# Kernel tuning notes

Measured on AMD Instinct MI355X. Metric: run time of the kernel, lower is better.

The kernel has to match this reference:

```python
import jax, jax.numpy as jnp
import numpy as np

D = 1024  # input_dim == output_dim
B = 4096  # batch (acts as sequence for batch-wise self-attention)


def setup_inputs() -> dict:
    key = jax.random.key(0)
    k1, k2, k3, k4 = jax.random.split(key, 4)
    inputs = jax.random.normal(k1, (B, D), dtype=jnp.float32)
    rotation_params = jax.random.normal(k2, (D, D), dtype=jnp.float32)
    # torch nn.Linear(input_dim, output_dim): weight (out, in), bias (out,)
    linear_w = jax.random.normal(k3, (D, D), dtype=jnp.float32) * (1.0 / np.sqrt(D))
    linear_b = jax.random.normal(k4, (D,), dtype=jnp.float32) * 0.01
    return {"inputs": inputs, "rotation_params": rotation_params,
            "linear_w": linear_w, "linear_b": linear_b}


def reference(inputs, rotation_params, linear_w, linear_b):
    # query = X R ; key = X R^T  -> scores = softmax(Q K^T / sqrt(D)) over batch dim
    query = inputs @ rotation_params                 # [B, D]
    key = inputs @ rotation_params.T                 # [B, D]
    scale = 1.0 / np.sqrt(D).astype(np.float32)
    scores = jax.nn.softmax(jnp.einsum('bd,cd->bc', query, key) * scale, axis=-1)  # [B, B]
    weighted = scores @ inputs                        # [B, D]
    return weighted @ linear_w.T + linear_b           # [B, out]
```

## Files before the change

### kernel.cpp

```cpp
#include <hip/hip_runtime.h>
#include <math.h>
#include <stdint.h>

using f16 = _Float16;
using half8 = __attribute__((ext_vector_type(8))) f16;
using half4 = __attribute__((ext_vector_type(4))) f16;
using f32x4 = __attribute__((ext_vector_type(4))) float;

__device__ __forceinline__ void gl_lds16(const f16* g, f16* l) {
  __builtin_amdgcn_global_load_lds(
      (const __attribute__((address_space(1))) void*)g,
      (__attribute__((address_space(3))) void*)l, 16, 0, 0);
}

__global__ __launch_bounds__(512, 2) void gemm_q3(
    const f16* __restrict__ Ap, const f16* __restrict__ Bp,
    f16* __restrict__ Ch, long sCp, int N, int K, long sAp, long sBp,
    float scale) {
  __shared__ f16 lds[2 * 4096 * 8];
  const int tid = threadIdx.x;
  const int lane = tid & 63;
  const int wave = tid >> 6;
  const int wr = (wave >> 2) * 128;
  const int wc = (wave & 3) * 64;

  const int nwg = gridDim.x * gridDim.y;
  int bid = blockIdx.y * gridDim.x + blockIdx.x;
  bid = (bid & 7) * (nwg >> 3) + (bid >> 3);
  const int bm = (bid / gridDim.x) * 256;
  const int bn = (bid % gridDim.x) * 256;

  const int nt = K / 32;

  auto stage = [&](int t, int i) {
    const int g0 = i * 512 + wave * 64;
    const int ga = g0 + lane;
    const bool isB = ga >= 2048;
    const int gl = ga & 2047;
    const int pl = gl >> 10;
    const int gp = gl & 1023;
    const int r = gp >> 2;
    const int cg = (gp & 3) ^ ((r >> 1) & 3);
    const f16* gs = (isB ? Bp + (size_t)pl * sBp + (size_t)(bn + r) * K
                         : Ap + (size_t)pl * sAp + (size_t)(bm + r) * K) +
                    t * 32 + cg * 8;
    gl_lds16(gs, &lds[((size_t)(t & 1) * 4096 + g0) * 8]);
  };

  int aoff[2][8], boff[2][4];
#pragma unroll
  for (int pl = 0; pl < 2; ++pl) {
#pragma unroll
    for (int fr = 0; fr < 8; ++fr) {
      const int row = wr + fr * 16 + (lane & 15);
      const int kg = (lane >> 4) ^ ((row >> 1) & 3);
      aoff[pl][fr] = (pl * 1024 + row * 4 + kg) * 8;
    }
#pragma unroll
    for (int fc = 0; fc < 4; ++fc) {
      const int col = wc + fc * 16 + (lane & 15);
      const int kg = (lane >> 4) ^ ((col >> 1) & 3);
      boff[pl][fc] = (2048 + pl * 1024 + col * 4 + kg) * 8;
    }
  }

  f32x4 acc[8][4];
#pragma unroll
  for (int m = 0; m < 8; ++m)
#pragma unroll
    for (int n = 0; n < 4; ++n) acc[m][n] = (f32x4){0.f, 0.f, 0.f, 0.f};

  half8 af0[2][4], af1[2][4], bf0[2][2], bf1[2][2];

#define LOAD_A(dst, h)                                          \
  _Pragma("unroll") for (int pl = 0; pl < 2; ++pl)              \
      _Pragma("unroll") for (int i = 0; i < 4; ++i) dst[pl][i] = \
          *(const half8*)&buf[aoff[pl][(h) * 4 + i]];
#define LOAD_B(dst, h)                                          \
  _Pragma("unroll") for (int pl = 0; pl < 2; ++pl)              \
      _Pragma("unroll") for (int j = 0; j < 2; ++j) dst[pl][j] = \
          *(const half8*)&buf[boff[pl][(h) * 2 + j]];
#define MFMA_Q(A, B, ah, bh)                                                  \
  _Pragma("unroll") for (int i = 0; i < 4; ++i)                               \
      _Pragma("unroll") for (int j = 0; j < 2; ++j) {                         \
    f32x4& c = acc[(ah) * 4 + i][(bh) * 2 + j];                               \
    c = __builtin_amdgcn_mfma_f32_16x16x32_f16(A[0][i], B[0][j], c, 0, 0, 0); \
    c = __builtin_amdgcn_mfma_f32_16x16x32_f16(A[0][i], B[1][j], c, 0, 0, 0); \
    c = __builtin_amdgcn_mfma_f32_16x16x32_f16(A[1][i], B[0][j], c, 0, 0, 0); \
  }
#define SBAR0() __builtin_amdgcn_sched_barrier(0)

#pragma unroll
  for (int i = 0; i < 8; ++i) stage(0, i);

  for (int t = 0; t < nt; ++t) {
    const f16* buf = &lds[(size_t)(t & 1) * 4096 * 8];
    asm volatile("s_barrier" ::: "memory");
    const bool pf = (t + 1 < nt);
    if (pf) {
      stage(t + 1, 0); stage(t + 1, 1); stage(t + 1, 2); stage(t + 1, 3);
      SBAR0();
      asm volatile("s_waitcnt vmcnt(4)" ::: "memory");
    } else {
      asm volatile("s_waitcnt vmcnt(0)" ::: "memory");
    }
    SBAR0();
    LOAD_A(af0, 0);
    LOAD_B(bf0, 0);
    LOAD_B(bf1, 1);
    SBAR0();
    __builtin_amdgcn_s_setprio(1);
    MFMA_Q(af0, bf0, 0, 0);
    __builtin_amdgcn_s_setprio(0);
    SBAR0();
    LOAD_A(af1, 1);
    if (pf) { stage(t + 1, 4); stage(t + 1, 5); stage(t + 1, 6); stage(t + 1, 7); }
    SBAR0();
    __builtin_amdgcn_s_setprio(1);
    MFMA_Q(af0, bf1, 0, 1);
    __builtin_amdgcn_s_setprio(0);
    SBAR0();
    LOAD_B(bf0, 0);
    SBAR0();
    __builtin_amdgcn_s_setprio(1);
    MFMA_Q(af1, bf1, 1, 1);
    __builtin_amdgcn_s_setprio(0);
    SBAR0();
    __builtin_amdgcn_s_setprio(1);
    MFMA_Q(af1, bf0, 1, 0);
    __builtin_amdgcn_s_setprio(0);
    SBAR0();
  }
#undef LOAD_A
#undef LOAD_B
#undef MFMA_Q
#undef SBAR0

#pragma unroll
  for (int m = 0; m < 8; ++m) {
#pragma unroll
    for (int n = 0; n < 4; ++n) {
      const int col = bn + wc + n * 16 + (lane & 15);
#pragma unroll
      for (int q = 0; q < 4; ++q) {
        const int row = bm + wr + m * 16 + (lane >> 4) * 4 + q;
        const float v = acc[m][n][q] * scale;
        const f16 h = (f16)v;
        Ch[(size_t)row * N + col] = h;
        Ch[sCp + (size_t)row * N + col] = (f16)(v - (float)h);
      }
    }
  }
}

template <int NP, int EPI, bool BIASF>
__global__ __launch_bounds__(512, 2) void gemm_dp(
    const f16* __restrict__ Ap, const f16* __restrict__ Bp,
    void* __restrict__ Cv, const float* __restrict__ bias, int M, int N, int K,
    long sAp, long sBp, long sCp, float scale) {
  __shared__ f16 lds[3 * 2048 * 8];
  const int tid = threadIdx.x;
  const int lane = tid & 63;
  const int wave = tid >> 6;
  const int wr = (wave >> 1) * 32;
  const int wc = (wave & 1) * 64;

  const int nwg = gridDim.x * gridDim.y;
  int bid = blockIdx.y * gridDim.x + blockIdx.x;
  bid = (bid & 7) * (nwg >> 3) + (bid >> 3);
  const int bm = (bid / gridDim.x) * 128;
  const int bn = (bid % gridDim.x) * 128;

  constexpr int KSTEP = (NP == 2) ? 32 : 64;
  const int nt = K / KSTEP;

  auto stage = [&](int t, int i) {
    const int g0 = i * 512 + wave * 64;
    const int ga = g0 + lane;
    const bool isB = ga >= 1024;
    const int gl = ga & 1023;
    const int pl = gl >> 9;
    const int gp = gl & 511;
    const int r = gp >> 2;
    const int cg = (gp & 3) ^ ((r >> 1) & 3);
    const long sP = (NP == 2) ? (isB ? sBp : sAp) : 0;
    const int kOff = (NP == 2) ? 0 : pl * 32;
    const f16* gs = (isB ? Bp : Ap) + (size_t)pl * sP +
                    (size_t)((isB ? bn : bm) + r) * K + t * KSTEP + kOff +
                    cg * 8;
    gl_lds16(gs, &lds[((size_t)(t % 3) * 2048 + g0) * 8]);
  };

  int aoff[2][2], boff[2][4];
#pragma unroll
  for (int pl = 0; pl < 2; ++pl) {
#pragma unroll
    for (int m = 0; m < 2; ++m) {
      const int row = wr + m * 16 + (lane & 15);
      const int kg = (lane >> 4) ^ ((row >> 1) & 3);
      aoff[pl][m] = (pl * 512 + row * 4 + kg) * 8;
    }
#pragma unroll
    for (int n = 0; n < 4; ++n) {
      const int col = wc + n * 16 + (lane & 15);
      const int kg = (lane >> 4) ^ ((col >> 1) & 3);
      boff[pl][n] = (1024 + pl * 512 + col * 4 + kg) * 8;
    }
  }

  f32x4 acc[2][4];
#pragma unroll
  for (int m = 0; m < 2; ++m)
#pragma unroll
    for (int n = 0; n < 4; ++n) acc[m][n] = (f32x4){0.f, 0.f, 0.f, 0.f};

#pragma unroll
  for (int i = 0; i < 4; ++i) stage(0, i);
#pragma unroll
  for (int i = 0; i < 4; ++i) stage(1, i);

  for (int t = 0; t < nt; ++t) {
    const f16* buf = &lds[(size_t)(t % 3) * 2048 * 8];
    if (t + 1 < nt)
      asm volatile("s_waitcnt vmcnt(4)" ::: "memory");
    else
      asm volatile("s_waitcnt vmcnt(0)" ::: "memory");
    asm volatile("s_barrier" ::: "memory");

    half8 af[2][2], b0[2][2];
#pragma unroll
    for (int pl = 0; pl < 2; ++pl) {
#pragma unroll
      for (int m = 0; m < 2; ++m) af[pl][m] = *(const half8*)&buf[aoff[pl][m]];
#pragma unroll
      for (int j = 0; j < 2; ++j) b0[pl][j] = *(const half8*)&buf[boff[pl][j]];
    }
    if (t + 2 < nt) {
      stage(t + 2, 0);
      stage(t + 2, 1);
    }
    __builtin_amdgcn_sched_barrier(0);
    asm volatile("s_barrier" ::: "memory");
    asm volatile("s_waitcnt lgkmcnt(0)" ::: "memory");
    __builtin_amdgcn_sched_barrier(0);
    __builtin_amdgcn_s_setprio(1);
#pragma unroll
    for (int m = 0; m < 2; ++m) {
#pragma unroll
      for (int j = 0; j < 2; ++j) {
        acc[m][j] = __builtin_amdgcn_mfma_f32_16x16x32_f16(af[0][m], b0[0][j],
                                                           acc[m][j], 0, 0, 0);
        if (NP == 2) {
          acc[m][j] = __builtin_amdgcn_mfma_f32_16x16x32_f16(
              af[0][m], b0[1][j], acc[m][j], 0, 0, 0);
          acc[m][j] = __builtin_amdgcn_mfma_f32_16x16x32_f16(
              af[1][m], b0[0][j], acc[m][j], 0, 0, 0);
        } else {
          acc[m][j] = __builtin_amdgcn_mfma_f32_16x16x32_f16(
              af[1][m], b0[1][j], acc[m][j], 0, 0, 0);
        }
      }
    }
    __builtin_amdgcn_s_setprio(0);
    __builtin_amdgcn_sched_barrier(0);
    asm volatile("s_barrier" ::: "memory");

    half8 b1[2][2];
#pragma unroll
    for (int pl = 0; pl < 2; ++pl)
#pragma unroll
      for (int j = 0; j < 2; ++j)
        b1[pl][j] = *(const half8*)&buf[boff[pl][2 + j]];
    if (t + 2 < nt) {
      stage(t + 2, 2);
      stage(t + 2, 3);
    }
    __builtin_amdgcn_sched_barrier(0);
    asm volatile("s_barrier" ::: "memory");
    asm volatile("s_waitcnt lgkmcnt(0)" ::: "memory");
    __builtin_amdgcn_sched_barrier(0);
    __builtin_amdgcn_s_setprio(1);
#pragma unroll
    for (int m = 0; m < 2; ++m) {
#pragma unroll
      for (int j = 0; j < 2; ++j) {
        acc[m][2 + j] = __builtin_amdgcn_mfma_f32_16x16x32_f16(
            af[0][m], b1[0][j], acc[m][2 + j], 0, 0, 0);
        if (NP == 2) {
          acc[m][2 + j] = __builtin_amdgcn_mfma_f32_16x16x32_f16(
              af[0][m], b1[1][j], acc[m][2 + j], 0, 0, 0);
          acc[m][2 + j] = __builtin_amdgcn_mfma_f32_16x16x32_f16(
              af[1][m], b1[0][j], acc[m][2 + j], 0, 0, 0);
        } else {
          acc[m][2 + j] = __builtin_amdgcn_mfma_f32_16x16x32_f16(
              af[1][m], b1[1][j], acc[m][2 + j], 0, 0, 0);
        }
      }
    }
    __builtin_amdgcn_s_setprio(0);
    __builtin_amdgcn_sched_barrier(0);
  }

#pragma unroll
  for (int m = 0; m < 2; ++m) {
#pragma unroll
    for (int n = 0; n < 4; ++n) {
      const int col = bn + wc + n * 16 + (lane & 15);
      const float bv = BIASF ? bias[col] : 0.f;
#pragma unroll
      for (int q = 0; q < 4; ++q) {
        const int row = bm + wr + m * 16 + (lane >> 4) * 4 + q;
        float v = acc[m][n][q] * scale;
        if (EPI == 0) {
          ((float*)Cv)[(size_t)row * N + col] = v + bv;
        } else if (EPI == 1) {
          f16* C = (f16*)Cv;
          const f16 h = (f16)v;
          C[(size_t)row * N + col] = h;
          C[sCp + (size_t)row * N + col] = (f16)(v - (float)h);
        } else {
          ((f16*)Cv)[(size_t)row * N + col] = (f16)v;
        }
      }
    }
  }
}

template <int NP, int TN, int EPI, bool BIASF, int MINW>
__global__ __launch_bounds__(256, MINW) void gemm_mp(
    const f16* __restrict__ Ap, const f16* __restrict__ Bp,
    void* __restrict__ Cv, const float* __restrict__ bias, int M, int N, int K,
    long sAp, long sBp, long sCp, float scale) {
  constexpr int FR = (TN == 128) ? 4 : 2;
  constexpr int FC = 4;
  constexpr int AG = NP * 512;
  constexpr int BPG = TN * 4;
  __shared__ f16 As[NP * 128 * 32];
  __shared__ f16 Bs[NP * TN * 32];
  const int tid = threadIdx.x;
  const int lane = tid & 63;
  const int wave = tid >> 6;
  const int wr = (TN == 128) ? (wave >> 1) * 64 : wave * 32;
  const int wc = (TN == 128) ? (wave & 1) * 64 : 0;

  const int nwg = gridDim.x * gridDim.y;
  int bid = blockIdx.y * gridDim.x + blockIdx.x;
  bid = (bid & 7) * (nwg >> 3) + (bid >> 3);
  const int bm = (bid / gridDim.x) * 128;
  const int bn = (bid % gridDim.x) * TN;

  int aoff[NP][FR], boff[NP][FC];
#pragma unroll
  for (int p = 0; p < NP; ++p) {
#pragma unroll
    for (int m = 0; m < FR; ++m) {
      const int row = wr + m * 16 + (lane & 15);
      const int kga = (lane >> 4) ^ ((row >> 1) & 3);
      aoff[p][m] = (p * 512 + row * 4 + kga) * 8;
    }
#pragma unroll
    for (int n = 0; n < FC; ++n) {
      const int col = wc + n * 16 + (lane & 15);
      const int kgb = (lane >> 4) ^ ((col >> 1) & 3);
      boff[p][n] = (p * BPG + col * 4 + kgb) * 8;
    }
  }

  f32x4 acc[FR][FC];
#pragma unroll
  for (int m = 0; m < FR; ++m)
#pragma unroll
    for (int n = 0; n < FC; ++n) acc[m][n] = (f32x4){0.f, 0.f, 0.f, 0.f};

  for (int k0 = 0; k0 < K; k0 += 32) {
#pragma unroll
    for (int i = 0; i < (NP * (512 + TN * 4)) / 256; ++i) {
      const int g0 = i * 256 + wave * 64;
      const bool isB = g0 >= AG;
      const int ga0 = g0 - (isB ? AG : 0);
      const int ga = ga0 + lane;
      const int pl = isB ? (ga / BPG) : (ga >> 9);
      const int gp = isB ? (ga % BPG) : (ga & 511);
      const int r = gp >> 2;
      const int cg = (gp & 3) ^ ((r >> 1) & 3);
      const f16* gs = (isB ? Bp + (size_t)pl * sBp + (size_t)(bn + r) * K
                           : Ap + (size_t)pl * sAp + (size_t)(bm + r) * K) +
                      k0 + cg * 8;
      f16* ld = (isB ? Bs : As) + (size_t)ga0 * 8;
      gl_lds16(gs, ld);
    }
    __syncthreads();

    half8 af[NP][FR], bf[NP][FC];
#pragma unroll
    for (int p = 0; p < NP; ++p) {
#pragma unroll
      for (int m = 0; m < FR; ++m) af[p][m] = *(const half8*)&As[aoff[p][m]];
#pragma unroll
      for (int n = 0; n < FC; ++n) bf[p][n] = *(const half8*)&Bs[boff[p][n]];
    }
#pragma unroll
    for (int m = 0; m < FR; ++m) {
#pragma unroll
      for (int n = 0; n < FC; ++n) {
        acc[m][n] = __builtin_amdgcn_mfma_f32_16x16x32_f16(af[0][m], bf[0][n],
                                                           acc[m][n], 0, 0, 0);
        if (NP == 2) {
          acc[m][n] = __builtin_amdgcn_mfma_f32_16x16x32_f16(
              af[0][m], bf[1][n], acc[m][n], 0, 0, 0);
          acc[m][n] = __builtin_amdgcn_mfma_f32_16x16x32_f16(
              af[1][m], bf[0][n], acc[m][n], 0, 0, 0);
        }
      }
    }
    __syncthreads();
  }

#pragma unroll
  for (int m = 0; m < FR; ++m) {
#pragma unroll
    for (int n = 0; n < FC; ++n) {
      const int col = bn + wc + n * 16 + (lane & 15);
      const float bv = BIASF ? bias[col] : 0.f;
#pragma unroll
      for (int q = 0; q < 4; ++q) {
        const int row = bm + wr + m * 16 + (lane >> 4) * 4 + q;
        float v = acc[m][n][q] * scale;
        if (EPI == 0) {
          ((float*)Cv)[(size_t)row * N + col] = v + bv;
        } else if (EPI == 1) {
          f16* C = (f16*)Cv;
          const f16 h = (f16)v;
          C[(size_t)row * N + col] = h;
          C[sCp + (size_t)row * N + col] = (f16)(v - (float)h);
        } else {
          ((f16*)Cv)[(size_t)row * N + col] = (f16)v;
        }
      }
    }
  }
}

template <int NP>
__global__ __launch_bounds__(256) void split_n(const float* __restrict__ in,
                                               f16* __restrict__ out,
                                               long planeStride, int n4) {
  const int i = blockIdx.x * 256 + threadIdx.x;
  if (i >= n4) return;
  const float4 v = ((const float4*)in)[i];
  const float vv[4] = {v.x, v.y, v.z, v.w};
  half4 h, mm;
#pragma unroll
  for (int q = 0; q < 4; ++q) {
    h[q] = (f16)vv[q];
    if (NP == 2) mm[q] = (f16)(vv[q] - (float)h[q]);
  }
  ((half4*)out)[i] = h;
  if (NP == 2) ((half4*)(out + planeStride))[i] = mm;
}

template <int NP>
__global__ __launch_bounds__(256) void split_t(const float* __restrict__ in,
                                               f16* __restrict__ out, int Mr,
                                               int Nc, long planeStride) {
  __shared__ float Ls[64][65];
  const int i0 = blockIdx.y * 64;
  const int j0 = blockIdx.x * 64;
  const int t = threadIdx.x;
  const int r = t >> 4;
  const int c = (t & 15) * 4;
#pragma unroll
  for (int i = 0; i < 4; ++i) {
    const float4 v =
        *(const float4*)&in[(size_t)(i0 + r + i * 16) * Nc + j0 + c];
    Ls[r + i * 16][c + 0] = v.x;
    Ls[r + i * 16][c + 1] = v.y;
    Ls[r + i * 16][c + 2] = v.z;
    Ls[r + i * 16][c + 3] = v.w;
  }
  __syncthreads();
#pragma unroll
  for (int i = 0; i < 4; ++i) {
    const int r2 = r + i * 16;
    half4 h, mm;
#pragma unroll
    for (int q = 0; q < 4; ++q) {
      const float v = Ls[c + q][r2];
      h[q] = (f16)v;
      if (NP == 2) mm[q] = (f16)(v - (float)h[q]);
    }
    *(half4*)&out[(size_t)(j0 + r2) * Mr + i0 + c] = h;
    if (NP == 2)
      *(half4*)&out[planeStride + (size_t)(j0 + r2) * Mr + i0 + c] = mm;
  }
}

__global__ __launch_bounds__(256) void softmax_ps(const f16* __restrict__ Lh,
                                                  long sL,
                                                  f16* __restrict__ P) {
  __shared__ float row[4096];
  __shared__ float red[8];
  const int rix = blockIdx.x;
  const f16* ph = Lh + (size_t)rix * 4096;
  const f16* pm = ph + sL;
  f16* o = P + (size_t)rix * 4096;
  const int tid = threadIdx.x;

  float mx = -INFINITY;
  for (int i = tid * 8; i < 4096; i += 2048) {
    const half8 h = *(const half8*)&ph[i];
    const half8 mseg = *(const half8*)&pm[i];
#pragma unroll
    for (int q = 0; q < 8; ++q) {
      const float v = (float)h[q] + (float)mseg[q];
      row[i + q] = v;
      mx = fmaxf(mx, v);
    }
  }
#pragma unroll
  for (int off = 32; off > 0; off >>= 1) mx = fmaxf(mx, __shfl_xor(mx, off));
  if ((tid & 63) == 0) red[tid >> 6] = mx;
  __syncthreads();
  mx = fmaxf(fmaxf(red[0], red[1]), fmaxf(red[2], red[3]));

  float s = 0.f;
  for (int i = tid * 4; i < 4096; i += 1024) {
    float4 v = *reinterpret_cast<const float4*>(&row[i]);
    v.x = expf(v.x - mx);
    v.y = expf(v.y - mx);
    v.z = expf(v.z - mx);
    v.w = expf(v.w - mx);
    s += v.x + v.y + v.z + v.w;
    *reinterpret_cast<float4*>(&row[i]) = v;
  }
#pragma unroll
  for (int off = 32; off > 0; off >>= 1) s += __shfl_xor(s, off);
  if ((tid & 63) == 0) red[4 + (tid >> 6)] = s;
  __syncthreads();
  s = red[4] + red[5] + red[6] + red[7];
  const float inv = 1.0f / s;

  for (int i = tid * 8; i < 4096; i += 2048) {
    half8 h;
#pragma unroll
    for (int q = 0; q < 8; ++q) h[q] = (f16)(row[i + q] * inv);
    *(half8*)&o[i] = h;
  }
}

extern "C" void kernel_launch(void* const* d_in, const int* in_sizes, int n_in,
                              void* d_out, int out_size, void* d_ws,
                              size_t ws_size, hipStream_t stream) {
  const float* X = (const float*)d_in[0];
  const float* R = (const float*)d_in[1];
  const float* Wl = (const float*)d_in[2];
  const float* bias = (const float*)d_in[3];
  float* out = (float*)d_out;

  const int Bq = 4096, D = 1024;
  const size_t MiB = 1 << 20;
  uint8_t* w8 = (uint8_t*)d_ws;
  f16* Xp = (f16*)(w8);
  f16* Tp = (f16*)(w8 + 16 * MiB);
  f16* Yt = (f16*)(w8 + 32 * MiB);
  f16* Wp = (f16*)(w8 + 40 * MiB);
  f16* Rp = (f16*)(w8 + 42 * MiB);
  f16* Rtp = (f16*)(w8 + 46 * MiB);
  f16* Mtp = (f16*)(w8 + 50 * MiB);
  f16* Lh = (f16*)(w8 + 54 * MiB);
  f16* Pp = (f16*)(w8);

  const long sR = (long)D * D, sX = (long)Bq * D;
  const long sL = (long)Bq * Bq;
  const dim3 blk(256), blk512(512);

  split_n<2><<<D * D / 1024, blk, 0, stream>>>(R, Rp, sR, D * D / 4);
  split_t<2><<<dim3(D / 64, D / 64), blk, 0, stream>>>(R, Rtp, D, D, sR);
  split_n<2><<<Bq * D / 1024, blk, 0, stream>>>(X, Xp, sX, Bq * D / 4);
  split_n<1><<<D * D / 1024, blk, 0, stream>>>(Wl, Wp, 0, D * D / 4);

  gemm_mp<2, 64, 1, false, 2><<<dim3(D / 64, D / 128), blk, 0, stream>>>(
      Rtp, Rp, Mtp, nullptr, D, D, D, sR, sR, sR, 1.f);
  gemm_dp<1, 2, false><<<dim3(Bq / 128, D / 128), blk512, 0, stream>>>(
      Wp, Xp, Yt, nullptr, D, Bq, D, 0, 0, 0, 1.f);
  gemm_dp<2, 1, false><<<dim3(D / 128, Bq / 128), blk512, 0, stream>>>(
      Xp, Mtp, Tp, nullptr, Bq, D, D, sX, sR, sX, 1.f);
  gemm_q3<<<dim3(Bq / 256, Bq / 256), blk512, 0, stream>>>(
      Tp, Xp, Lh, sL, Bq, D, sX, sX, 0.03125f);
  softmax_ps<<<dim3(Bq), blk, 0, stream>>>(Lh, sL, Pp);
  gemm_dp<1, 0, true><<<dim3(D / 128, Bq / 128), blk512, 0, stream>>>(
      Pp, Yt, out, bias, Bq, D, Bq, 0, 0, 0, 1.f);
}
```

Baseline: 241.2 us.

## Restructure score GEMM main loop into per-plane phases; fuse split kernels

The three-plane score GEMM loop now works one precision-plane product at a time across the full 8x4 fragment tile. It spreads the next tile's global-to-LDS stages across three phases with finer vmcnt waits and extra barriers, aiming for better overlap of loads with MFMA work. Three of the fp32-to-fp16 split kernels are merged into one launch to cut launch overhead. In exchange the loop carries more barriers per iteration and relies on hand-tuned waitcnt values, which could race if the counts are wrong.

```diff
diff --git a/kernel.cpp b/kernel.cpp
--- a/kernel.cpp
+++ b/kernel.cpp
@@ -13,7 +13,7 @@
       (__attribute__((address_space(3))) void*)l, 16, 0, 0);
 }
 
-__global__ __launch_bounds__(512, 2) void gemm_q3(
+__global__ __launch_bounds__(512, 2) void gemm_q4(
     const f16* __restrict__ Ap, const f16* __restrict__ Bp,
     f16* __restrict__ Ch, long sCp, int N, int K, long sAp, long sBp,
     float scale) {
@@ -32,8 +32,8 @@
 
   const int nt = K / 32;
 
-  auto stage = [&](int t, int i) {
-    const int g0 = i * 512 + wave * 64;
+  auto stage = [&](int t, int c) {
+    const int g0 = c * 512 + wave * 64;
     const int ga = g0 + lane;
     const bool isB = ga >= 2048;
     const int gl = ga & 2047;
@@ -70,70 +70,78 @@
 #pragma unroll
     for (int n = 0; n < 4; ++n) acc[m][n] = (f32x4){0.f, 0.f, 0.f, 0.f};
 
-  half8 af0[2][4], af1[2][4], bf0[2][2], bf1[2][2];
-
-#define LOAD_A(dst, h)                                          \
-  _Pragma("unroll") for (int pl = 0; pl < 2; ++pl)              \
-      _Pragma("unroll") for (int i = 0; i < 4; ++i) dst[pl][i] = \
-          *(const half8*)&buf[aoff[pl][(h) * 4 + i]];
-#define LOAD_B(dst, h)                                          \
-  _Pragma("unroll") for (int pl = 0; pl < 2; ++pl)              \
-      _Pragma("unroll") for (int j = 0; j < 2; ++j) dst[pl][j] = \
-          *(const half8*)&buf[boff[pl][(h) * 2 + j]];
-#define MFMA_Q(A, B, ah, bh)                                                  \
-  _Pragma("unroll") for (int i = 0; i < 4; ++i)                               \
-      _Pragma("unroll") for (int j = 0; j < 2; ++j) {                         \
-    f32x4& c = acc[(ah) * 4 + i][(bh) * 2 + j];                               \
-    c = __builtin_amdgcn_mfma_f32_16x16x32_f16(A[0][i], B[0][j], c, 0, 0, 0); \
-    c = __builtin_amdgcn_mfma_f32_16x16x32_f16(A[0][i], B[1][j], c, 0, 0, 0); \
-    c = __builtin_amdgcn_mfma_f32_16x16x32_f16(A[1][i], B[0][j], c, 0, 0, 0); \
-  }
+  half8 a0[8], a1[8], b0[4], b1[4];
+
+#define RD_A(dst, pl)                                   \
+  _Pragma("unroll") for (int i = 0; i < 8; ++i) dst[i] = \
+      *(const half8*)&buf[aoff[pl][i]];
+#define RD_B(dst, pl)                                   \
+  _Pragma("unroll") for (int j = 0; j < 4; ++j) dst[j] = \
+      *(const half8*)&buf[boff[pl][j]];
+#define MFMA_P(A, B)                                                        \
+  _Pragma("unroll") for (int i = 0; i < 8; ++i)                             \
+      _Pragma("unroll") for (int j = 0; j < 4; ++j) acc[i][j] =             \
+          __builtin_amdgcn_mfma_f32_16x16x32_f16(A[i], B[j], acc[i][j], 0, \
+                                                 0, 0);
 #define SBAR0() __builtin_amdgcn_sched_barrier(0)
 
-#pragma unroll
-  for (int i = 0; i < 8; ++i) stage(0, i);
+  stage(0, 0); stage(0, 1); stage(0, 4); stage(0, 5);
+  stage(0, 6); stage(0, 7); stage(0, 2); stage(0, 3);
+  asm volatile("s_waitcnt vmcnt(4)" ::: "memory");
+  asm volatile("s_barrier" ::: "memory");
 
   for (int t = 0; t < nt; ++t) {
     const f16* buf = &lds[(size_t)(t & 1) * 4096 * 8];
+    const bool pf = (t + 1 < nt);
+
+    RD_A(a0, 0);
+    RD_B(b0, 0);
+    if (pf) { stage(t + 1, 0); stage(t + 1, 1); stage(t + 1, 4); }
+    SBAR0();
+    asm volatile("s_waitcnt lgkmcnt(0)" ::: "memory");
+    SBAR0();
+    __builtin_amdgcn_s_setprio(1);
+    MFMA_P(a0, b0);
+    __builtin_amdgcn_s_setprio(0);
+    SBAR0();
+    if (pf)
+      asm volatile("s_waitcnt vmcnt(5)" ::: "memory");
+    else
+      asm volatile("s_waitcnt vmcnt(2)" ::: "memory");
     asm volatile("s_barrier" ::: "memory");
-    const bool pf = (t + 1 < nt);
-    if (pf) {
-      stage(t + 1, 0); stage(t + 1, 1); stage(t + 1, 2); stage(t + 1, 3);
-      SBAR0();
+
+    RD_B(b1, 1);
+    if (pf) { stage(t + 1, 5); stage(t + 1, 6); stage(t + 1, 7); }
+    SBAR0();
+    asm volatile("s_waitcnt lgkmcnt(0)" ::: "memory");
+    SBAR0();
+    __builtin_amdgcn_s_setprio(1);
+    MFMA_P(a0, b1);
+    __builtin_amdgcn_s_setprio(0);
+    SBAR0();
+    if (pf)
+      asm volatile("s_waitcnt vmcnt(6)" ::: "memory");
+    else
+      asm volatile("s_waitcnt vmcnt(0)" ::: "memory");
+    asm volatile("s_barrier" ::: "memory");
+
+    RD_A(a1, 1);
+    RD_B(b0, 0);
+    if (pf) { stage(t + 1, 2); stage(t + 1, 3); }
+    SBAR0();
+    asm volatile("s_waitcnt lgkmcnt(0)" ::: "memory");
+    SBAR0();
+    __builtin_amdgcn_s_setprio(1);
+    MFMA_P(a1, b0);
+    __builtin_amdgcn_s_setprio(0);
+    SBAR0();
+    if (pf)
       asm volatile("s_waitcnt vmcnt(4)" ::: "memory");
-    } else {
-      asm volatile("s_waitcnt vmcnt(0)" ::: "memory");
-    }
-    SBAR0();
-    LOAD_A(af0, 0);
-    LOAD_B(bf0, 0);
-    LOAD_B(bf1, 1);
-    SBAR0();
-    __builtin_amdgcn_s_setprio(1);
-    MFMA_Q(af0, bf0, 0, 0);
-    __builtin_amdgcn_s_setprio(0);
-    SBAR0();
-    LOAD_A(af1, 1);
-    if (pf) { stage(t + 1, 4); stage(t + 1, 5); stage(t + 1, 6); stage(t + 1, 7); }
-    SBAR0();
-    __builtin_amdgcn_s_setprio(1);
-    MFMA_Q(af0, bf1, 0, 1);
-    __builtin_amdgcn_s_setprio(0);
-    SBAR0();
-    LOAD_B(bf0, 0);
-    SBAR0();
-    __builtin_amdgcn_s_setprio(1);
-    MFMA_Q(af1, bf1, 1, 1);
-    __builtin_amdgcn_s_setprio(0);
-    SBAR0();
-    __builtin_amdgcn_s_setprio(1);
-    MFMA_Q(af1, bf0, 1, 0);
-    __builtin_amdgcn_s_setprio(0);
-    SBAR0();
-  }
-#undef LOAD_A
-#undef LOAD_B
-#undef MFMA_Q
+    asm volatile("s_barrier" ::: "memory");
+  }
+#undef RD_A
+#undef RD_B
+#undef MFMA_P
 #undef SBAR0
 
 #pragma unroll
@@ -441,28 +449,37 @@
   }
 }
 
-template <int NP>
-__global__ __launch_bounds__(256) void split_n(const float* __restrict__ in,
-                                               f16* __restrict__ out,
-                                               long planeStride, int n4) {
-  const int i = blockIdx.x * 256 + threadIdx.x;
-  if (i >= n4) return;
+__global__ __launch_bounds__(256) void split_fused(
+    const float* __restrict__ X, const float* __restrict__ R,
+    const float* __restrict__ W, f16* __restrict__ Xp, f16* __restrict__ Rp,
+    f16* __restrict__ Wp, long sX, long sR) {
+  const int b = blockIdx.x;
+  const float* in;
+  f16* out;
+  long ps;
+  int np, i;
+  if (b < 4096) {
+    in = X; out = Xp; ps = sX; np = 2; i = b * 256 + threadIdx.x;
+  } else if (b < 5120) {
+    in = R; out = Rp; ps = sR; np = 2; i = (b - 4096) * 256 + threadIdx.x;
+  } else {
+    in = W; out = Wp; ps = 0; np = 1; i = (b - 5120) * 256 + threadIdx.x;
+  }
   const float4 v = ((const float4*)in)[i];
   const float vv[4] = {v.x, v.y, v.z, v.w};
   half4 h, mm;
 #pragma unroll
   for (int q = 0; q < 4; ++q) {
     h[q] = (f16)vv[q];
-    if (NP == 2) mm[q] = (f16)(vv[q] - (float)h[q]);
+    mm[q] = (f16)(vv[q] - (float)h[q]);
   }
   ((half4*)out)[i] = h;
-  if (NP == 2) ((half4*)(out + planeStride))[i] = mm;
-}
-
-template <int NP>
-__global__ __launch_bounds__(256) void split_t(const float* __restrict__ in,
-                                               f16* __restrict__ out, int Mr,
-                                               int Nc, long planeStride) {
+  if (np == 2) ((half4*)(out + ps))[i] = mm;
+}
+
+__global__ __launch_bounds__(256) void split_t2(const float* __restrict__ in,
+                                                f16* __restrict__ out, int Mr,
+                                                int Nc, long planeStride) {
   __shared__ float Ls[64][65];
   const int i0 = blockIdx.y * 64;
   const int j0 = blockIdx.x * 64;
@@ -487,11 +504,10 @@
     for (int q = 0; q < 4; ++q) {
       const float v = Ls[c + q][r2];
       h[q] = (f16)v;
-      if (NP == 2) mm[q] = (f16)(v - (float)h[q]);
+      mm[q] = (f16)(v - (float)h[q]);
     }
     *(half4*)&out[(size_t)(j0 + r2) * Mr + i0 + c] = h;
-    if (NP == 2)
-      *(half4*)&out[planeStride + (size_t)(j0 + r2) * Mr + i0 + c] = mm;
+    *(half4*)&out[planeStride + (size_t)(j0 + r2) * Mr + i0 + c] = mm;
   }
 }
 
@@ -574,10 +590,8 @@
   const long sL = (long)Bq * Bq;
   const dim3 blk(256), blk512(512);
 
-  split_n<2><<<D * D / 1024, blk, 0, stream>>>(R, Rp, sR, D * D / 4);
-  split_t<2><<<dim3(D / 64, D / 64), blk, 0, stream>>>(R, Rtp, D, D, sR);
-  split_n<2><<<Bq * D / 1024, blk, 0, stream>>>(X, Xp, sX, Bq * D / 4);
-  split_n<1><<<D * D / 1024, blk, 0, stream>>>(Wl, Wp, 0, D * D / 4);
+  split_fused<<<dim3(6144), blk, 0, stream>>>(X, R, Wl, Xp, Rp, Wp, sX, sR);
+  split_t2<<<dim3(D / 64, D / 64), blk, 0, stream>>>(R, Rtp, D, D, sR);
 
   gemm_mp<2, 64, 1, false, 2><<<dim3(D / 64, D / 128), blk, 0, stream>>>(
       Rtp, Rp, Mtp, nullptr, D, D, D, sR, sR, sR, 1.f);
@@ -585,7 +599,7 @@
       Wp, Xp, Yt, nullptr, D, Bq, D, 0, 0, 0, 1.f);
   gemm_dp<2, 1, false><<<dim3(D / 128, Bq / 128), blk512, 0, stream>>>(
       Xp, Mtp, Tp, nullptr, Bq, D, D, sX, sR, sX, 1.f);
-  gemm_q3<<<dim3(Bq / 256, Bq / 256), blk512, 0, stream>>>(
+  gemm_q4<<<dim3(Bq / 256, Bq / 256), blk512, 0, stream>>>(
       Tp, Xp, Lh, sL, Bq, D, sX, sX, 0.03125f);
   softmax_ps<<<dim3(Bq), blk, 0, stream>>>(Lh, sL, Pp);
   gemm_dp<1, 0, true><<<dim3(D / 128, Bq / 128), blk512, 0, stream>>>(
```

Result: slower. 403.8 us (+67.4%).

## Reorder logits GEMM prefetch after LDS reads and fuse split kernels

Applied to the files above, without the earlier changes.

The big logits GEMM now waits for all outstanding global loads at the start of each iteration, then issues the first half of the next-tile prefetch after the first LDS fragment reads, instead of prefetching before them and waiting on a partial vmcnt. The three non-transposed fp32-to-fp16 split launches are merged into one kernel that picks its source by block index. This cuts launch overhead but exposes full global-load latency at each iteration boundary. It also risks a race, since the prefetch of the next tile may write the LDS buffer other waves are still reading.

```diff
diff --git a/kernel.cpp b/kernel.cpp
--- a/kernel.cpp
+++ b/kernel.cpp
@@ -13,7 +13,7 @@
       (__attribute__((address_space(3))) void*)l, 16, 0, 0);
 }
 
-__global__ __launch_bounds__(512, 2) void gemm_q3(
+__global__ __launch_bounds__(512, 2) void gemm_q2(
     const f16* __restrict__ Ap, const f16* __restrict__ Bp,
     f16* __restrict__ Ch, long sCp, int N, int K, long sAp, long sBp,
     float scale) {
@@ -95,18 +95,14 @@
 
   for (int t = 0; t < nt; ++t) {
     const f16* buf = &lds[(size_t)(t & 1) * 4096 * 8];
+    asm volatile("s_waitcnt vmcnt(0)" ::: "memory");
     asm volatile("s_barrier" ::: "memory");
     const bool pf = (t + 1 < nt);
-    if (pf) {
-      stage(t + 1, 0); stage(t + 1, 1); stage(t + 1, 2); stage(t + 1, 3);
-      SBAR0();
-      asm volatile("s_waitcnt vmcnt(4)" ::: "memory");
-    } else {
-      asm volatile("s_waitcnt vmcnt(0)" ::: "memory");
-    }
-    SBAR0();
+
     LOAD_A(af0, 0);
     LOAD_B(bf0, 0);
+    if (pf) { stage(t + 1, 0); stage(t + 1, 1); stage(t + 1, 2); stage(t + 1, 3); }
+    SBAR0();
     LOAD_B(bf1, 1);
     SBAR0();
     __builtin_amdgcn_s_setprio(1);
@@ -441,28 +437,37 @@
   }
 }
 
-template <int NP>
-__global__ __launch_bounds__(256) void split_n(const float* __restrict__ in,
-                                               f16* __restrict__ out,
-                                               long planeStride, int n4) {
-  const int i = blockIdx.x * 256 + threadIdx.x;
-  if (i >= n4) return;
+__global__ __launch_bounds__(256) void split_fused(
+    const float* __restrict__ X, const float* __restrict__ R,
+    const float* __restrict__ W, f16* __restrict__ Xp, f16* __restrict__ Rp,
+    f16* __restrict__ Wp, long sX, long sR) {
+  const int b = blockIdx.x;
+  const float* in;
+  f16* out;
+  long ps;
+  int np, i;
+  if (b < 4096) {
+    in = X; out = Xp; ps = sX; np = 2; i = b * 256 + threadIdx.x;
+  } else if (b < 5120) {
+    in = R; out = Rp; ps = sR; np = 2; i = (b - 4096) * 256 + threadIdx.x;
+  } else {
+    in = W; out = Wp; ps = 0; np = 1; i = (b - 5120) * 256 + threadIdx.x;
+  }
   const float4 v = ((const float4*)in)[i];
   const float vv[4] = {v.x, v.y, v.z, v.w};
   half4 h, mm;
 #pragma unroll
   for (int q = 0; q < 4; ++q) {
     h[q] = (f16)vv[q];
-    if (NP == 2) mm[q] = (f16)(vv[q] - (float)h[q]);
+    mm[q] = (f16)(vv[q] - (float)h[q]);
   }
   ((half4*)out)[i] = h;
-  if (NP == 2) ((half4*)(out + planeStride))[i] = mm;
-}
-
-template <int NP>
-__global__ __launch_bounds__(256) void split_t(const float* __restrict__ in,
-                                               f16* __restrict__ out, int Mr,
-                                               int Nc, long planeStride) {
+  if (np == 2) ((half4*)(out + ps))[i] = mm;
+}
+
+__global__ __launch_bounds__(256) void split_t2(const float* __restrict__ in,
+                                                f16* __restrict__ out, int Mr,
+                                                int Nc, long planeStride) {
   __shared__ float Ls[64][65];
   const int i0 = blockIdx.y * 64;
   const int j0 = blockIdx.x * 64;
@@ -487,11 +492,10 @@
     for (int q = 0; q < 4; ++q) {
       const float v = Ls[c + q][r2];
       h[q] = (f16)v;
-      if (NP == 2) mm[q] = (f16)(v - (float)h[q]);
+      mm[q] = (f16)(v - (float)h[q]);
     }
     *(half4*)&out[(size_t)(j0 + r2) * Mr + i0 + c] = h;
-    if (NP == 2)
-      *(half4*)&out[planeStride + (size_t)(j0 + r2) * Mr + i0 + c] = mm;
+    *(half4*)&out[planeStride + (size_t)(j0 + r2) * Mr + i0 + c] = mm;
   }
 }
 
@@ -574,10 +578,8 @@
   const long sL = (long)Bq * Bq;
   const dim3 blk(256), blk512(512);
 
-  split_n<2><<<D * D / 1024, blk, 0, stream>>>(R, Rp, sR, D * D / 4);
-  split_t<2><<<dim3(D / 64, D / 64), blk, 0, stream>>>(R, Rtp, D, D, sR);
-  split_n<2><<<Bq * D / 1024, blk, 0, stream>>>(X, Xp, sX, Bq * D / 4);
-  split_n<1><<<D * D / 1024, blk, 0, stream>>>(Wl, Wp, 0, D * D / 4);
+  split_fused<<<dim3(6144), blk, 0, stream>>>(X, R, Wl, Xp, Rp, Wp, sX, sR);
+  split_t2<<<dim3(D / 64, D / 64), blk, 0, stream>>>(R, Rtp, D, D, sR);
 
   gemm_mp<2, 64, 1, false, 2><<<dim3(D / 64, D / 128), blk, 0, stream>>>(
       Rtp, Rp, Mtp, nullptr, D, D, D, sR, sR, sR, 1.f);
@@ -585,7 +587,7 @@
       Wp, Xp, Yt, nullptr, D, Bq, D, 0, 0, 0, 1.f);
   gemm_dp<2, 1, false><<<dim3(D / 128, Bq / 128), blk512, 0, stream>>>(
       Xp, Mtp, Tp, nullptr, Bq, D, D, sX, sR, sX, 1.f);
-  gemm_q3<<<dim3(Bq / 256, Bq / 256), blk512, 0, stream>>>(
+  gemm_q2<<<dim3(Bq / 256, Bq / 256), blk512, 0, stream>>>(
       Tp, Xp, Lh, sL, Bq, D, sX, sX, 0.03125f);
   softmax_ps<<<dim3(Bq), blk, 0, stream>>>(Lh, sL, Pp);
   gemm_dp<1, 0, true><<<dim3(D / 128, Bq / 128), blk512, 0, stream>>>(
```

New measurement: 235.5 us. -2.4%, faster.
